# Kernel tuning notes

Hardware: AMD Instinct MI355X
Metric: run time of the kernel (lower is better)

The kernel has to match this reference:

```python
import jax, jax.numpy as jnp
import numpy as np

NUM_HEADS = 16
DIM_K = 128
DIM_V = 128
ROPE_BASE = 10000.0


def rope(x):
    # x: [..., seq, d]; rotate-half convention
    d = x.shape[-1]
    seq = x.shape[-2]
    half = d // 2
    inv_freq = 1.0 / (ROPE_BASE ** (jnp.arange(0, half, dtype=jnp.float32) / half))
    ang = jnp.arange(seq, dtype=jnp.float32)[:, None] * inv_freq[None, :]  # [seq, half]
    cos, sin = jnp.cos(ang), jnp.sin(ang)
    x1, x2 = x[..., :half], x[..., half:]
    return jnp.concatenate([x1 * cos - x2 * sin, x1 * sin + x2 * cos], axis=-1)


def setup_inputs() -> dict:
    key = jax.random.key(0)
    ks = jax.random.split(key, 8)
    B, S, D = 2, 2048, 2048
    s = lambda fan_in: 1.0 / np.sqrt(fan_in)
    return {
        'q_in': jax.random.normal(ks[0], (B, S, D), jnp.float32),
        'k_in': jax.random.normal(ks[1], (B, S, D), jnp.float32),
        'v_in': jax.random.normal(ks[2], (B, S, D), jnp.float32),
        'mask': jnp.zeros((B, S), dtype=bool),
        'Wq': jax.random.normal(ks[3], (D, NUM_HEADS * DIM_K), jnp.float32) * s(D),
        'bq': jnp.zeros((NUM_HEADS * DIM_K,), jnp.float32),
        'Wk': jax.random.normal(ks[4], (D, DIM_K), jnp.float32) * s(D),
        'bk': jnp.zeros((DIM_K,), jnp.float32),
        'Wv': jax.random.normal(ks[5], (D, DIM_V), jnp.float32) * s(D),
        'bv': jnp.zeros((DIM_V,), jnp.float32),
        'Wo': jax.random.normal(ks[6], (NUM_HEADS * DIM_V, D), jnp.float32) * s(NUM_HEADS * DIM_V),
        'bo': jnp.zeros((D,), jnp.float32),
    }


def reference(q_in, k_in, v_in, mask, Wq, bq, Wk, bk, Wv, bv, Wo, bo):
    B, Sq, _ = q_in.shape
    Sk = k_in.shape[1]
    # projections: multi-head Q, single shared K/V head (MQA)
    q = (q_in @ Wq + bq).reshape(B, Sq, NUM_HEADS, DIM_K).transpose(0, 2, 1, 3)  # [B,H,Sq,dk]
    k = k_in @ Wk + bk  # [B,Sk,dk]
    v = v_in @ Wv + bv  # [B,Sk,dv]
    # inline RoPE on q and k
    q = rope(q)
    k = rope(k)
    scores = jnp.einsum('bhqd,bkd->bhqk', q, k) / np.sqrt(DIM_K)  # [B,H,Sq,Sk]
    # padding mask: True means masked out
    scores = jnp.where(mask[:, None, None, :], -jnp.inf, scores)
    # causal mask
    causal = jnp.triu(jnp.ones((Sq, Sk), dtype=bool), k=1)
    scores = jnp.where(causal[None, None], -jnp.inf, scores)
    weights = jax.nn.softmax(scores, axis=-1)
    attn = jnp.einsum('bhqk,bkd->bhqd', weights, v)  # [B,H,Sq,dv]
    attn = attn.transpose(0, 2, 1, 3).reshape(B, Sq, NUM_HEADS * DIM_V)
    return attn @ Wo + bo
```

## Files before the change

kernel.cpp:

```cpp
#include <hip/hip_runtime.h>

#define NHEADS 16
#define DKV 128
#define BB 2
#define SS 2048
#define DD 2048

typedef __attribute__((ext_vector_type(8))) short bf16x8;
typedef __attribute__((ext_vector_type(4))) short bf16x4;
typedef __attribute__((ext_vector_type(4))) float f32x4;
typedef __attribute__((ext_vector_type(8))) _Float16 f16x8;

#define QSCL 0.12752775f

__device__ __forceinline__ short f2bf(float x) {
  unsigned u = __builtin_bit_cast(unsigned, x);
  unsigned r = (u + 0x7fffu + ((u >> 16) & 1u)) >> 16;
  return (short)(unsigned short)r;
}
__device__ __forceinline__ float bf2f(short s) {
  unsigned u = ((unsigned)(unsigned short)s) << 16;
  return __builtin_bit_cast(float, u);
}
__device__ __forceinline__ unsigned pk2bf(float a, float b) {
#if __has_builtin(__builtin_amdgcn_cvt_pk_bf16_f32)
  typedef __attribute__((ext_vector_type(2))) __bf16 bf2_t;
  bf2_t r = __builtin_amdgcn_cvt_pk_bf16_f32(a, b);
  return __builtin_bit_cast(unsigned, r);
#else
  unsigned ua = __builtin_bit_cast(unsigned, a);
  unsigned ub = __builtin_bit_cast(unsigned, b);
  return ((ua + 0x8000u) >> 16) | ((ub + 0x8000u) & 0xffff0000u);
#endif
}
__device__ __forceinline__ unsigned pkf16(float a, float b) {
#if __has_builtin(__builtin_amdgcn_cvt_pkrtz)
  typedef __attribute__((ext_vector_type(2))) __fp16 h2_t;
  h2_t r = __builtin_amdgcn_cvt_pkrtz(a, b);
  return __builtin_bit_cast(unsigned, r);
#else
  _Float16 ha = (_Float16)a, hb = (_Float16)b;
  unsigned short ua = __builtin_bit_cast(unsigned short, ha);
  unsigned short ub = __builtin_bit_cast(unsigned short, hb);
  return (unsigned)ua | ((unsigned)ub << 16);
#endif
}
__device__ __forceinline__ float exp2fast(float x) {
#if __has_builtin(__builtin_amdgcn_exp2f)
  return __builtin_amdgcn_exp2f(x);
#else
  return exp2f(x);
#endif
}

__device__ __forceinline__ void async16(const void* g, void* l) {
  __builtin_amdgcn_global_load_lds(
      (__attribute__((address_space(1))) void*)g,
      (__attribute__((address_space(3))) void*)l, 16, 0, 0);
}

__global__ __launch_bounds__(256) void prep(
    const float* __restrict__ q_in, short* __restrict__ qb,
    const float* __restrict__ Wq, short* __restrict__ Wqt,
    const float* __restrict__ Wo, short* __restrict__ Wot,
    const float* __restrict__ Wk, short* __restrict__ Wkt,
    const float* __restrict__ Wv, short* __restrict__ Wvt) {
  const int id = blockIdx.x;
  if (id < 4096) {
    int idx = id * 256 + threadIdx.x;
    int g = idx * 8;
    float4 a = *(const float4*)(q_in + g);
    float4 b = *(const float4*)(q_in + g + 4);
    uint4 o = {pk2bf(a.x, a.y), pk2bf(a.z, a.w), pk2bf(b.x, b.y),
               pk2bf(b.z, b.w)};
    *(uint4*)(qb + g) = o;
    return;
  }
  __shared__ float T[32][33];
  const float* W;
  short* Wt;
  float scale = 1.0f;
  int N, bx, by;
  if (id < 12288) {
    int Lt = id - 4096;
    int z = Lt >> 12;
    int rem = Lt & 4095;
    bx = rem & 63;
    by = rem >> 6;
    N = DD;
    if (z == 0) { W = Wq; Wt = Wqt; scale = QSCL; }
    else        { W = Wo; Wt = Wot; }
  } else {
    int Ls = id - 12288;
    int z = Ls >> 8;
    int rem = Ls & 255;
    bx = rem & 3;
    by = rem >> 2;
    N = DKV;
    if (z == 0) { W = Wk; Wt = Wkt; }
    else        { W = Wv; Wt = Wvt; }
  }
  const int K = DD;
  const int nt = bx * 32;
  const int kt = by * 32;
  const int tx = threadIdx.x & 31;
  const int ty = threadIdx.x >> 5;
#pragma unroll
  for (int i = 0; i < 4; ++i)
    T[ty + i * 8][tx] = W[(size_t)(kt + ty + i * 8) * N + nt + tx];
  __syncthreads();
#pragma unroll
  for (int i = 0; i < 4; ++i)
    Wt[(size_t)(nt + ty + i * 8) * K + kt + tx] = f2bf(T[tx][ty + i * 8] * scale);
}

template <int AMODE>
__global__ __launch_bounds__(256) void gemm_as(
    const void* __restrict__ Ap, const short* __restrict__ Bt,
    const float* __restrict__ bias, void* __restrict__ Cp,
    int M, int N, int K, int KC, int cmode, float bscale) {
  __shared__ __align__(16) short As[128 * 32];
  __shared__ __align__(16) short Bs[128 * 32];
  const int tid = threadIdx.x;
  int bxi = blockIdx.x, byi = blockIdx.y;
  if (gridDim.x == 16 && gridDim.y == 32) {
    int L = byi * 16 + bxi;
    int i = L & 7, t = L >> 3;
    byi = 8 * (i >> 1) + (t & 7);
    bxi = 2 * (t >> 3) + (i & 1);
  }
  const int bm = byi * 128;
  const int bn = bxi * 128;
  const int kz = blockIdx.z;
  const int w = tid >> 6, lane = tid & 63;
  const int lm = lane & 15, q4 = lane >> 4;
  const int m0 = (w & 1) * 64, n0 = (w >> 1) * 64;

  f32x4 acc[4][4];
#pragma unroll
  for (int mi = 0; mi < 4; ++mi)
#pragma unroll
    for (int ni = 0; ni < 4; ++ni) acc[mi][ni] = (f32x4){0.f, 0.f, 0.f, 0.f};

  const int kbeg = kz * KC;
  const int kend = kbeg + KC;

  for (int k0 = kbeg; k0 < kend; k0 += 32) {
    __syncthreads();
    if (AMODE == 1) {
      const short* Ab = (const short*)Ap;
#pragma unroll
      for (int i = 0; i < 2; ++i) {
        int rA = (w * 2 + i) * 16 + (lane >> 2);
        int cA = (lane & 3) ^ (rA & 3);
        async16(Ab + (size_t)(bm + rA) * K + k0 + cA * 8, &As[(w * 2 + i) * 512]);
      }
    } else {
      const float* Af = (const float*)Ap;
      float4 av[4];
#pragma unroll
      for (int i = 0; i < 4; ++i) {
        int qd = tid + i * 256;
        int r = qd >> 3, cq = qd & 7;
        av[i] = *(const float4*)(Af + (size_t)(bm + r) * K + k0 + cq * 4);
      }
#pragma unroll
      for (int i = 0; i < 4; ++i) {
        int qd = tid + i * 256;
        int r = qd >> 3, cq = qd & 7;
        int ch = cq >> 1, hf = cq & 1;
        int pc = ch ^ (r & 3);
        bf16x4 t = {f2bf(av[i].x), f2bf(av[i].y), f2bf(av[i].z), f2bf(av[i].w)};
        *(bf16x4*)&As[r * 32 + pc * 8 + hf * 4] = t;
      }
    }
#pragma unroll
    for (int i = 0; i < 2; ++i) {
      int rB = (w * 2 + i) * 16 + (lane >> 2);
      int cB = (lane & 3) ^ (rB & 3);
      async16(Bt + (size_t)(bn + rB) * K + k0 + cB * 8, &Bs[(w * 2 + i) * 512]);
    }
    __syncthreads();

    bf16x8 af[4], bf[4];
#pragma unroll
    for (int mi = 0; mi < 4; ++mi)
      af[mi] = *(const bf16x8*)&As[(m0 + mi * 16 + lm) * 32 + ((q4 ^ (lm & 3)) * 8)];
#pragma unroll
    for (int ni = 0; ni < 4; ++ni)
      bf[ni] = *(const bf16x8*)&Bs[(n0 + ni * 16 + lm) * 32 + ((q4 ^ (lm & 3)) * 8)];
#pragma unroll
    for (int mi = 0; mi < 4; ++mi)
#pragma unroll
      for (int ni = 0; ni < 4; ++ni)
        acc[mi][ni] = __builtin_amdgcn_mfma_f32_16x16x32_bf16(
            af[mi], bf[ni], acc[mi][ni], 0, 0, 0);
  }

  if (cmode == 2) {
    float* Cf = (float*)Cp + (size_t)kz * M * N;
#pragma unroll
    for (int mi = 0; mi < 4; ++mi)
#pragma unroll
      for (int ni = 0; ni < 4; ++ni)
#pragma unroll
        for (int reg = 0; reg < 4; ++reg)
          Cf[(size_t)(bm + m0 + mi * 16 + q4 * 4 + reg) * N +
             (bn + n0 + ni * 16 + lm)] = acc[mi][ni][reg];
  } else {
#pragma unroll
    for (int mi = 0; mi < 4; ++mi)
#pragma unroll
      for (int ni = 0; ni < 4; ++ni)
#pragma unroll
        for (int reg = 0; reg < 4; ++reg) {
          int rowg = bm + m0 + mi * 16 + q4 * 4 + reg;
          int colg = bn + n0 + ni * 16 + lm;
          float val = acc[mi][ni][reg] + bias[colg] * bscale;
          if (cmode == 0)
            ((float*)Cp)[(size_t)rowg * N + colg] = val;
          else
            ((short*)Cp)[(size_t)rowg * N + colg] = f2bf(val);
        }
  }
}

#define SPLITK 4
__global__ __launch_bounds__(256) void gemm_qkv(
    const float* __restrict__ k_in, const float* __restrict__ v_in,
    const short* __restrict__ Btk, const short* __restrict__ Btv,
    float* __restrict__ kpart, float* __restrict__ vpart,
    const short* __restrict__ qb, const short* __restrict__ Wqt,
    const float* __restrict__ bq, short* __restrict__ qp) {
  __shared__ __align__(16) short As[128 * 32];
  __shared__ __align__(16) short Bs[128 * 32];
  const int tid = threadIdx.x;
  const int w = tid >> 6, lane = tid & 63;
  const int lm = lane & 15, q4 = lane >> 4;
  const int m0 = (w & 1) * 64, n0 = (w >> 1) * 64;
  const int id = blockIdx.x;

  f32x4 acc[4][4];
#pragma unroll
  for (int mi = 0; mi < 4; ++mi)
#pragma unroll
    for (int ni = 0; ni < 4; ++ni) acc[mi][ni] = (f32x4){0.f, 0.f, 0.f, 0.f};

  if (id < 256) {
    const int ym = id & 31, zz = id >> 5;
    const int kz = zz & 3;
    const float* Af = (zz >= 4) ? v_in : k_in;
    const short* Bt = (zz >= 4) ? Btv : Btk;
    float* Cf = ((zz >= 4) ? vpart : kpart) + (size_t)kz * (4096 * 128);
    const int bm = ym * 128;
    const int K = DD, N = DKV;
    const int kbeg = kz * (DD / SPLITK);
    const int kend = kbeg + DD / SPLITK;

    for (int k0 = kbeg; k0 < kend; k0 += 32) {
      __syncthreads();
      {
        float4 av[4];
#pragma unroll
        for (int i = 0; i < 4; ++i) {
          int qd = tid + i * 256;
          int r = qd >> 3, cq = qd & 7;
          av[i] = *(const float4*)(Af + (size_t)(bm + r) * K + k0 + cq * 4);
        }
#pragma unroll
        for (int i = 0; i < 4; ++i) {
          int qd = tid + i * 256;
          int r = qd >> 3, cq = qd & 7;
          int ch = cq >> 1, hf = cq & 1;
          int pc = ch ^ (r & 3);
          bf16x4 t = {f2bf(av[i].x), f2bf(av[i].y), f2bf(av[i].z), f2bf(av[i].w)};
          *(bf16x4*)&As[r * 32 + pc * 8 + hf * 4] = t;
        }
      }
#pragma unroll
      for (int i = 0; i < 2; ++i) {
        int rB = (w * 2 + i) * 16 + (lane >> 2);
        int cB = (lane & 3) ^ (rB & 3);
        async16(Bt + (size_t)rB * K + k0 + cB * 8, &Bs[(w * 2 + i) * 512]);
      }
      __syncthreads();

      bf16x8 af[4], bf[4];
#pragma unroll
      for (int mi = 0; mi < 4; ++mi)
        af[mi] = *(const bf16x8*)&As[(m0 + mi * 16 + lm) * 32 + ((q4 ^ (lm & 3)) * 8)];
#pragma unroll
      for (int ni = 0; ni < 4; ++ni)
        bf[ni] = *(const bf16x8*)&Bs[(n0 + ni * 16 + lm) * 32 + ((q4 ^ (lm & 3)) * 8)];
#pragma unroll
      for (int mi = 0; mi < 4; ++mi)
#pragma unroll
        for (int ni = 0; ni < 4; ++ni)
          acc[mi][ni] = __builtin_amdgcn_mfma_f32_16x16x32_bf16(
              af[mi], bf[ni], acc[mi][ni], 0, 0, 0);
    }

#pragma unroll
    for (int mi = 0; mi < 4; ++mi)
#pragma unroll
      for (int ni = 0; ni < 4; ++ni)
#pragma unroll
        for (int reg = 0; reg < 4; ++reg)
          Cf[(size_t)(bm + m0 + mi * 16 + q4 * 4 + reg) * N +
             (n0 + ni * 16 + lm)] = acc[mi][ni][reg];
  } else {
    int L = id - 256;
    int i2 = L & 7, t2 = L >> 3;
    const int byi = 8 * (i2 >> 1) + (t2 & 7);
    const int bxi = 2 * (t2 >> 3) + (i2 & 1);
    const int bm = byi * 128;
    const int bn = bxi * 128;
    const int K = DD, N = DD;

    for (int k0 = 0; k0 < DD; k0 += 32) {
      __syncthreads();
#pragma unroll
      for (int i = 0; i < 2; ++i) {
        int rA = (w * 2 + i) * 16 + (lane >> 2);
        int cA = (lane & 3) ^ (rA & 3);
        async16(qb + (size_t)(bm + rA) * K + k0 + cA * 8, &As[(w * 2 + i) * 512]);
      }
#pragma unroll
      for (int i = 0; i < 2; ++i) {
        int rB = (w * 2 + i) * 16 + (lane >> 2);
        int cB = (lane & 3) ^ (rB & 3);
        async16(Wqt + (size_t)(bn + rB) * K + k0 + cB * 8, &Bs[(w * 2 + i) * 512]);
      }
      __syncthreads();

      bf16x8 af[4], bf[4];
#pragma unroll
      for (int mi = 0; mi < 4; ++mi)
        af[mi] = *(const bf16x8*)&As[(m0 + mi * 16 + lm) * 32 + ((q4 ^ (lm & 3)) * 8)];
#pragma unroll
      for (int ni = 0; ni < 4; ++ni)
        bf[ni] = *(const bf16x8*)&Bs[(n0 + ni * 16 + lm) * 32 + ((q4 ^ (lm & 3)) * 8)];
#pragma unroll
      for (int mi = 0; mi < 4; ++mi)
#pragma unroll
        for (int ni = 0; ni < 4; ++ni)
          acc[mi][ni] = __builtin_amdgcn_mfma_f32_16x16x32_bf16(
              af[mi], bf[ni], acc[mi][ni], 0, 0, 0);
    }

#pragma unroll
    for (int mi = 0; mi < 4; ++mi)
#pragma unroll
      for (int ni = 0; ni < 4; ++ni)
#pragma unroll
        for (int reg = 0; reg < 4; ++reg) {
          int rowg = bm + m0 + mi * 16 + q4 * 4 + reg;
          int colg = bn + n0 + ni * 16 + lm;
          qp[(size_t)rowg * N + colg] =
              f2bf(acc[mi][ni][reg] + bq[colg] * QSCL);
        }
  }
}

__global__ __launch_bounds__(256) void kv_reduce(
    const float* __restrict__ kpart, const float* __restrict__ vpart,
    const float* __restrict__ bk, const float* __restrict__ bv,
    short* __restrict__ kp, short* __restrict__ vtb,
    const unsigned char* __restrict__ m, float* __restrict__ mb) {
  __shared__ float Kt[16][128];
  __shared__ short Vl[128][18];
  const int tid = threadIdx.x;
  const int r0 = blockIdx.x * 16;
  if (tid < 16) mb[r0 + tid] = m[r0 + tid] ? -1e30f : 0.0f;
#pragma unroll
  for (int i = 0; i < 8; ++i) {
    int e = tid + i * 256;
    int r = e >> 7, c = e & 127;
    float sk = 0.f, sv = 0.f;
#pragma unroll
    for (int z = 0; z < SPLITK; ++z) {
      sk += kpart[((size_t)z * 4096 + r0 + r) * 128 + c];
      sv += vpart[((size_t)z * 4096 + r0 + r) * 128 + c];
    }
    Kt[r][c] = sk + bk[c];
    Vl[c][r] = f2bf(sv + bv[c]);
  }
  __syncthreads();
#pragma unroll
  for (int i = 0; i < 4; ++i) {
    int e = tid + i * 256;
    int r = e >> 6, d = e & 63;
    float x1 = Kt[r][d], x2 = Kt[r][d + 64];
    float s = (float)((r0 + r) & (SS - 1));
    float ang = s * exp2fast((float)d * (-13.287712379549449f / 64.0f));
    float sn, cs;
    __sincosf(ang, &sn, &cs);
    kp[(size_t)(r0 + r) * 128 + d] = f2bf(x1 * cs - x2 * sn);
    kp[(size_t)(r0 + r) * 128 + d + 64] = f2bf(x1 * sn + x2 * cs);
  }
  const int b = r0 >> 11;
  const int j = tid >> 1, soff = (tid & 1) * 8;
  short* dst = vtb + ((size_t)b * 128 + j) * SS + (r0 & (SS - 1)) + soff;
  bf16x8 tmp;
#pragma unroll
  for (int u = 0; u < 8; ++u) tmp[u] = Vl[j][soff + u];
  *(bf16x8*)dst = tmp;
}

#define PSTR 40

__global__ __launch_bounds__(512, 4) void flash_kernel(
    const short* __restrict__ q, const short* __restrict__ k,
    const short* __restrict__ vt, const float* __restrict__ mb,
    short* __restrict__ out, short* __restrict__ pO, float* __restrict__ pL) {
  __shared__ __align__(16) short Kb[2][32 * 128];
  __shared__ __align__(16) short Vb[2][128 * 64];
  __shared__ __align__(16) short Ps[8][16 * PSTR];
  const int j = blockIdx.x;
  const int cls = j >> 5, hb = j & 31;
  int qx, c;
  if (cls < 8) {
    qx = cls + 8; c = 0;
  } else {
    int kk = (cls - 8) >> 1;
    if ((cls & 1) == 0) { qx = 15 - kk; c = 1; }
    else                { qx = 7 - kk;  c = 0; }
  }
  const int h = hb & 15, b = hb >> 4;
  const int kt0 = c ? 32 : 0;
  int kend = 4 * qx + 4;
  if (c == 0 && kend > 32) kend = 32;

  const int tid = threadIdx.x;
  const int w = tid >> 6, lane = tid & 63;
  const int lm = lane & 15, q4 = lane >> 4;
  const int qrow0 = qx * 128 + w * 16;

  bf16x8 qf[4];
#pragma unroll
  for (int ks = 0; ks < 4; ++ks)
    qf[ks] = *(const bf16x8*)(q +
        ((size_t)b * SS + qrow0 + lm) * (NHEADS * DKV) + h * DKV +
        ks * 32 + q4 * 8);
  {
    float s = (float)(qrow0 + lm);
#pragma unroll
    for (int ks = 0; ks < 2; ++ks) {
      bf16x8 x1 = qf[ks], x2 = qf[ks + 2];
      bf16x8 y1, y2;
#pragma unroll
      for (int jj = 0; jj < 8; ++jj) {
        int d = ks * 32 + q4 * 8 + jj;
        float ang = s * exp2fast((float)d * (-13.287712379549449f / 64.0f));
        float sn, cs;
        __sincosf(ang, &sn, &cs);
        float a = bf2f(x1[jj]), b2 = bf2f(x2[jj]);
        y1[jj] = f2bf(a * cs - b2 * sn);
        y2[jj] = f2bf(a * sn + b2 * cs);
      }
      qf[ks] = y1;
      qf[ks + 2] = y2;
    }
  }

  bf16x8 onesb;
#pragma unroll
  for (int jj = 0; jj < 8; ++jj) onesb[jj] = (short)0x3F80;

  f32x4 O[8], Ol;
#pragma unroll
  for (int vi = 0; vi < 8; ++vi) O[vi] = (f32x4){0.f, 0.f, 0.f, 0.f};
  Ol = (f32x4){0.f, 0.f, 0.f, 0.f};

  const size_t kbase = (size_t)b * SS;

  {
    {
      int r = w * 4 + (lane >> 4);
      int cc = (lane & 15) ^ (r & 7);
      async16(k + (kbase + (size_t)kt0 * 32 + r) * DKV + cc * 8,
              &Kb[0][w * 512]);
    }
#pragma unroll
    for (int i = 0; i < 2; ++i) {
      int rV = (w * 2 + i) * 8 + (lane >> 3);
      int cV = (lane & 7) ^ (rV & 7);
      async16(vt + ((size_t)b * DKV + rV) * SS + (size_t)kt0 * 32 + cV * 8,
              &Vb[0][(w * 2 + i) * 512]);
    }
  }
  f32x4 mc0 = *(const f32x4*)(mb + kbase + (size_t)kt0 * 32 + q4 * 4);
  f32x4 mc1 = *(const f32x4*)(mb + kbase + (size_t)kt0 * 32 + 16 + q4 * 4);

  for (int kt = kt0; kt < kend; ++kt) {
    __syncthreads();

    f32x4 mn0, mn1;
    if (kt + 1 < kend) {
      const int t = kt + 1;
      {
        int r = w * 4 + (lane >> 4);
        int cc = (lane & 15) ^ (r & 7);
        async16(k + (kbase + (size_t)t * 32 + r) * DKV + cc * 8,
                &Kb[t & 1][w * 512]);
      }
      if (kt & 1) {
#pragma unroll
        for (int i = 0; i < 2; ++i) {
          int rV = (w * 2 + i) * 8 + (lane >> 3);
          int cV = (lane & 7) ^ (rV & 7);
          async16(vt + ((size_t)b * DKV + rV) * SS + (size_t)t * 32 + cV * 8,
                  &Vb[(t >> 1) & 1][(w * 2 + i) * 512]);
        }
      }
      mn0 = *(const f32x4*)(mb + kbase + (size_t)t * 32 + q4 * 4);
      mn1 = *(const f32x4*)(mb + kbase + (size_t)t * 32 + 16 + q4 * 4);
    }

    const short* Kc = Kb[kt & 1];
    f32x4 sacc[2];
#pragma unroll
    for (int mi = 0; mi < 2; ++mi) sacc[mi] = (f32x4){0.f, 0.f, 0.f, 0.f};
#pragma unroll
    for (int mi = 0; mi < 2; ++mi)
#pragma unroll
      for (int ks = 0; ks < 4; ++ks) {
        bf16x8 kf = *(const bf16x8*)&Kc[(mi * 16 + lm) * 128 +
                                        (((ks * 4 + q4) ^ (lm & 7)) << 3)];
        sacc[mi] = __builtin_amdgcn_mfma_f32_16x16x32_bf16(
            kf, qf[ks], sacc[mi], 0, 0, 0);
      }

    const bool diag = (kt >= 4 * qx);
#pragma unroll
    for (int mi = 0; mi < 2; ++mi) {
      f32x4 mbv = mi ? mc1 : mc0;
      float pv[4];
#pragma unroll
      for (int reg = 0; reg < 4; ++reg) {
        float s = sacc[mi][reg] + mbv[reg];
        if (diag) {
          int kg = kt * 32 + mi * 16 + q4 * 4 + reg;
          int qg = qrow0 + lm;
          if (kg > qg) s = -1e30f;
        }
        pv[reg] = exp2fast(s);
      }
      uint2 pkd = {pk2bf(pv[0], pv[1]), pk2bf(pv[2], pv[3])};
      *(uint2*)&Ps[w][lm * PSTR + mi * 16 + q4 * 4] = pkd;
    }
    mc0 = mn0;
    mc1 = mn1;

    const short* Vc = Vb[(kt >> 1) & 1];
    const int hf4 = (kt & 1) * 4;
    bf16x8 pf = *(const bf16x8*)&Ps[w][lm * PSTR + q4 * 8];
    Ol = __builtin_amdgcn_mfma_f32_16x16x32_bf16(pf, onesb, Ol, 0, 0, 0);
#pragma unroll
    for (int vi = 0; vi < 8; ++vi) {
      bf16x8 vf = *(const bf16x8*)&Vc[(vi * 16 + lm) * 64 +
                                      (((hf4 + q4) ^ (lm & 7)) << 3)];
      O[vi] = __builtin_amdgcn_mfma_f32_16x16x32_bf16(pf, vf, O[vi], 0, 0, 0);
    }
  }

  __syncthreads();
  float* Wr = (float*)&Vb[0][0] + w * 544;
  float linv[4];
#pragma unroll
  for (int reg = 0; reg < 4; ++reg) linv[reg] = 1.0f / Ol[reg];

  const bool split = (qx >= 8);
  short* obase;
  int ostr;
  if (split) {
    int slot = ((b * 16 + h) * 8 + (qx - 8)) * 2 + c;
    obase = pO + (size_t)slot * (128 * 128);
    ostr = 128;
    if (lm == 0) {
      float* dl = pL + (size_t)slot * 128 + w * 16;
#pragma unroll
      for (int reg = 0; reg < 4; ++reg)
        dl[q4 * 4 + reg] = Ol[reg];
    }
  } else {
    obase = out + ((size_t)b * SS + qx * 128) * (NHEADS * DKV) + h * DKV;
    ostr = NHEADS * DKV;
  }

#pragma unroll
  for (int qd = 0; qd < 4; ++qd) {
#pragma unroll
    for (int v2 = 0; v2 < 2; ++v2) {
      int vi = qd * 2 + v2;
#pragma unroll
      for (int reg = 0; reg < 4; ++reg)
        Wr[(q4 * 4 + reg) * 34 + v2 * 16 + lm] = O[vi][reg] * linv[reg];
    }
    int r = lane & 15, hh = lane >> 4;
    f32x4 t0 = *(const f32x4*)&Wr[r * 34 + hh * 8];
    f32x4 t1 = *(const f32x4*)&Wr[r * 34 + hh * 8 + 4];
    size_t oaddr = (size_t)(w * 16 + r) * ostr + qd * 32 + hh * 8;
    uint4 o0;
    if (split) {
      o0 = (uint4){pkf16(t0[0], t0[1]), pkf16(t0[2], t0[3]),
                   pkf16(t1[0], t1[1]), pkf16(t1[2], t1[3])};
    } else {
      o0 = (uint4){pk2bf(t0[0], t0[1]), pk2bf(t0[2], t0[3]),
                   pk2bf(t1[0], t1[1]), pk2bf(t1[2], t1[3])};
    }
    *(uint4*)(obase + oaddr) = o0;
  }
}

__global__ __launch_bounds__(256) void combine(
    const short* __restrict__ pO, const float* __restrict__ pL,
    short* __restrict__ out) {
  const int qxi = blockIdx.x, h = blockIdx.y, b = blockIdx.z;
  const int qx = 8 + qxi;
  const int slot2 = ((b * 16 + h) * 8 + qxi) * 2;
  const _Float16* p0 = (const _Float16*)(pO + (size_t)slot2 * (128 * 128));
  const _Float16* p1 = p0 + 128 * 128;
  const float* l0 = pL + (size_t)slot2 * 128;
  const float* l1 = l0 + 128;
  const int t = threadIdx.x;
  const int row = t >> 1, half = t & 1;
  const float w0 = l0[row], w1 = l1[row];
  const float inv = 1.0f / (w0 + w1);
  const float a0 = w0 * inv, a1 = w1 * inv;
  const int off = row * 128 + half * 64;
  short* dst = out + ((size_t)(b * SS + qx * 128 + row)) * (NHEADS * DKV) +
               h * DKV + half * 64;
#pragma unroll
  for (int v = 0; v < 8; ++v) {
    f16x8 x0 = *(const f16x8*)(p0 + off + v * 8);
    f16x8 x1 = *(const f16x8*)(p1 + off + v * 8);
    float r[8];
#pragma unroll
    for (int u = 0; u < 8; ++u)
      r[u] = (float)x0[u] * a0 + (float)x1[u] * a1;
    uint4 o = {pk2bf(r[0], r[1]), pk2bf(r[2], r[3]),
               pk2bf(r[4], r[5]), pk2bf(r[6], r[7])};
    *(uint4*)(dst + v * 8) = o;
  }
}

extern "C" void kernel_launch(void* const* d_in, const int* in_sizes, int n_in,
                              void* d_out, int out_size, void* d_ws, size_t ws_size,
                              hipStream_t stream) {
  const float* q_in = (const float*)d_in[0];
  const float* k_in = (const float*)d_in[1];
  const float* v_in = (const float*)d_in[2];
  const unsigned char* mask = (const unsigned char*)d_in[3];
  const float* Wq = (const float*)d_in[4];
  const float* bq = (const float*)d_in[5];
  const float* Wk = (const float*)d_in[6];
  const float* bk = (const float*)d_in[7];
  const float* Wv = (const float*)d_in[8];
  const float* bv = (const float*)d_in[9];
  const float* Wo = (const float*)d_in[10];
  const float* bo = (const float*)d_in[11];

  const int M = BB * SS;
  short* Wqt = (short*)d_ws;
  short* Wot = Wqt + (size_t)DD * DD;
  short* Wkt = Wot + (size_t)DD * DD;
  short* Wvt = Wkt + (size_t)DKV * DD;
  short* qb  = Wvt + (size_t)DKV * DD;
  short* qp  = qb + (size_t)M * DD;
  short* kp  = qp + (size_t)M * DD;
  short* vtb = kp + (size_t)M * DKV;
  float* mb  = (float*)(vtb + (size_t)BB * DKV * SS);
  float* kpart = mb + (size_t)BB * SS;
  float* vpart = kpart + (size_t)SPLITK * M * DKV;
  float* pL = vpart + (size_t)SPLITK * M * DKV;
  short* ap = qb;
  short* pO = (short*)kpart;

  prep<<<12800, 256, 0, stream>>>(q_in, qb, Wq, Wqt, Wo, Wot, Wk, Wkt, Wv, Wvt);

  gemm_qkv<<<768, 256, 0, stream>>>(k_in, v_in, Wkt, Wvt, kpart, vpart,
                                    qb, Wqt, bq, qp);
  kv_reduce<<<M / 16, 256, 0, stream>>>(kpart, vpart, bk, bv, kp, vtb, mask, mb);

  flash_kernel<<<dim3(768), 512, 0, stream>>>(qp, kp, vtb, mb, ap, pO, pL);
  combine<<<dim3(8, NHEADS, BB), 256, 0, stream>>>(pO, pL, ap);

  gemm_as<1><<<dim3(DD / 128, M / 128, 1), 256, 0, stream>>>(
      ap, Wot, bo, d_out, M, DD, DD, DD, 0, 1.0f);
}
```

Baseline: 363.4 us.

## Split-K the Q and output projections into two fp16 partials plus reduce kernels

The Q projection inside gemm_qkv and the final output GEMM are each split along K into two halves. Each half writes fp16 partial results, and a new qo_reduce kernel sums the two partials, adds the bias and writes bf16 or fp32. Doubling the block count is meant to fill the GPU better, since a 512-block GEMM gives few waves per CU. In exchange it adds extra memory traffic for the partials, two extra launches, and fp16 rounding of the partial sums, with a possible overflow risk. It also relies on qp being safe to reuse as the output partial buffer, and on the partial regions being large enough.

```diff
diff --git a/kernel.cpp b/kernel.cpp
--- a/kernel.cpp
+++ b/kernel.cpp
@@ -21,6 +21,10 @@
 __device__ __forceinline__ float bf2f(short s) {
   unsigned u = ((unsigned)(unsigned short)s) << 16;
   return __builtin_bit_cast(float, u);
+}
+__device__ __forceinline__ short f2h(float x) {
+  _Float16 h = (_Float16)x;
+  return __builtin_bit_cast(short, h);
 }
 __device__ __forceinline__ unsigned pk2bf(float a, float b) {
 #if __has_builtin(__builtin_amdgcn_cvt_pk_bf16_f32)
@@ -197,7 +201,17 @@
             af[mi], bf[ni], acc[mi][ni], 0, 0, 0);
   }
 
-  if (cmode == 2) {
+  if (cmode == 3) {
+    short* Ch = (short*)Cp + (size_t)kz * M * N;
+#pragma unroll
+    for (int mi = 0; mi < 4; ++mi)
+#pragma unroll
+      for (int ni = 0; ni < 4; ++ni)
+#pragma unroll
+        for (int reg = 0; reg < 4; ++reg)
+          Ch[(size_t)(bm + m0 + mi * 16 + q4 * 4 + reg) * N +
+             (bn + n0 + ni * 16 + lm)] = f2h(acc[mi][ni][reg]);
+  } else if (cmode == 2) {
     float* Cf = (float*)Cp + (size_t)kz * M * N;
 #pragma unroll
     for (int mi = 0; mi < 4; ++mi)
@@ -231,7 +245,7 @@
     const short* __restrict__ Btk, const short* __restrict__ Btv,
     float* __restrict__ kpart, float* __restrict__ vpart,
     const short* __restrict__ qb, const short* __restrict__ Wqt,
-    const float* __restrict__ bq, short* __restrict__ qp) {
+    short* __restrict__ qpart0, short* __restrict__ qpart1) {
   __shared__ __align__(16) short As[128 * 32];
   __shared__ __align__(16) short Bs[128 * 32];
   const int tid = threadIdx.x;
@@ -310,14 +324,18 @@
              (n0 + ni * 16 + lm)] = acc[mi][ni][reg];
   } else {
     int L = id - 256;
-    int i2 = L & 7, t2 = L >> 3;
+    const int kz = L >> 9;
+    int L2 = L & 511;
+    int i2 = L2 & 7, t2 = L2 >> 3;
     const int byi = 8 * (i2 >> 1) + (t2 & 7);
     const int bxi = 2 * (t2 >> 3) + (i2 & 1);
     const int bm = byi * 128;
     const int bn = bxi * 128;
     const int K = DD, N = DD;
-
-    for (int k0 = 0; k0 < DD; k0 += 32) {
+    const int kbeg = kz * 1024;
+    const int kend = kbeg + 1024;
+
+    for (int k0 = kbeg; k0 < kend; k0 += 32) {
       __syncthreads();
 #pragma unroll
       for (int i = 0; i < 2; ++i) {
@@ -348,17 +366,40 @@
               af[mi], bf[ni], acc[mi][ni], 0, 0, 0);
     }
 
+    short* dst = kz ? qpart1 : qpart0;
 #pragma unroll
     for (int mi = 0; mi < 4; ++mi)
 #pragma unroll
       for (int ni = 0; ni < 4; ++ni)
 #pragma unroll
-        for (int reg = 0; reg < 4; ++reg) {
-          int rowg = bm + m0 + mi * 16 + q4 * 4 + reg;
-          int colg = bn + n0 + ni * 16 + lm;
-          qp[(size_t)rowg * N + colg] =
-              f2bf(acc[mi][ni][reg] + bq[colg] * QSCL);
-        }
+        for (int reg = 0; reg < 4; ++reg)
+          dst[(size_t)(bm + m0 + mi * 16 + q4 * 4 + reg) * N +
+              (bn + n0 + ni * 16 + lm)] = f2h(acc[mi][ni][reg]);
+  }
+}
+
+template <int OUT32>
+__global__ __launch_bounds__(256) void qo_reduce(
+    const short* __restrict__ p0, const short* __restrict__ p1,
+    const float* __restrict__ bias, float bscale, void* __restrict__ outp) {
+  int idx = blockIdx.x * 256 + threadIdx.x;
+  int g = idx * 8;
+  f16x8 a = *(const f16x8*)(p0 + g);
+  f16x8 b = *(const f16x8*)(p1 + g);
+  int col = g & (DD - 1);
+  float r[8];
+#pragma unroll
+  for (int u = 0; u < 8; ++u)
+    r[u] = (float)a[u] + (float)b[u] + bias[col + u] * bscale;
+  if (OUT32) {
+    float4 o0 = {r[0], r[1], r[2], r[3]};
+    float4 o1 = {r[4], r[5], r[6], r[7]};
+    *(float4*)((float*)outp + g) = o0;
+    *(float4*)((float*)outp + g + 4) = o1;
+  } else {
+    uint4 o = {pk2bf(r[0], r[1]), pk2bf(r[2], r[3]),
+               pk2bf(r[4], r[5]), pk2bf(r[6], r[7])};
+    *(uint4*)((short*)outp + g) = o;
   }
 }
 
@@ -674,18 +715,23 @@
   float* kpart = mb + (size_t)BB * SS;
   float* vpart = kpart + (size_t)SPLITK * M * DKV;
   float* pL = vpart + (size_t)SPLITK * M * DKV;
+  short* xpart = (short*)(pL + (size_t)512 * 128);
   short* ap = qb;
   short* pO = (short*)kpart;
+  short* opart = qp;
 
   prep<<<12800, 256, 0, stream>>>(q_in, qb, Wq, Wqt, Wo, Wot, Wk, Wkt, Wv, Wvt);
 
-  gemm_qkv<<<768, 256, 0, stream>>>(k_in, v_in, Wkt, Wvt, kpart, vpart,
-                                    qb, Wqt, bq, qp);
+  gemm_qkv<<<1280, 256, 0, stream>>>(k_in, v_in, Wkt, Wvt, kpart, vpart,
+                                     qb, Wqt, qp, xpart);
+  qo_reduce<0><<<M * DD / 2048, 256, 0, stream>>>(qp, xpart, bq, QSCL, qp);
   kv_reduce<<<M / 16, 256, 0, stream>>>(kpart, vpart, bk, bv, kp, vtb, mask, mb);
 
   flash_kernel<<<dim3(768), 512, 0, stream>>>(qp, kp, vtb, mb, ap, pO, pL);
   combine<<<dim3(8, NHEADS, BB), 256, 0, stream>>>(pO, pL, ap);
 
-  gemm_as<1><<<dim3(DD / 128, M / 128, 1), 256, 0, stream>>>(
-      ap, Wot, bo, d_out, M, DD, DD, DD, 0, 1.0f);
-}
+  gemm_as<1><<<dim3(16, 32, 2), 256, 0, stream>>>(
+      ap, Wot, nullptr, opart, M, DD, DD, DD / 2, 3, 1.0f);
+  qo_reduce<1><<<M * DD / 2048, 256, 0, stream>>>(
+      opart, opart + (size_t)M * DD, bo, 1.0f, d_out);
+}
```

After: 381.8 us. +5.1%, slower.
